# Kernel tuning notes

Measured on AMD Instinct MI355X. Metric: run time of the kernel, lower is better.

## Reference

```python
import jax, jax.numpy as jnp
import numpy as np
from math import sqrt

INPUT, HIDDEN, OUTPUT = 256, 512, 256
B, T = 64, 1024


def setup_inputs() -> dict:
    key = jax.random.key(0)
    k1, k2, k3, k4 = jax.random.split(key, 4)
    x = jax.random.normal(k1, (B, T, INPUT), dtype=jnp.float32)
    W_xh = jax.random.normal(k2, (INPUT, HIDDEN), dtype=jnp.float32) * sqrt(2.0 / (INPUT + HIDDEN))
    W_hh = jax.random.normal(k3, (HIDDEN, HIDDEN), dtype=jnp.float32) * sqrt(1.0 / HIDDEN)
    b_h = jnp.zeros((HIDDEN,), dtype=jnp.float32)
    W_hy = jax.random.normal(k4, (HIDDEN, OUTPUT), dtype=jnp.float32) * sqrt(2.0 / (HIDDEN + OUTPUT))
    b_y = jnp.zeros((OUTPUT,), dtype=jnp.float32)
    return {"x": x, "W_xh": W_xh, "W_hh": W_hh, "b_h": b_h, "W_hy": W_hy, "b_y": b_y}


def reference(x, W_xh, W_hh, b_h, W_hy, b_y):
    # Precompute input projection for all timesteps: [B,T,H_in] @ [H_in,H] -> [B,T,H]
    xh = jnp.einsum('bti,ih->bth', x, W_xh) + b_h
    h0 = jnp.zeros((x.shape[0], W_hh.shape[0]), dtype=x.dtype)

    def step(h, xh_t):
        h_new = jnp.tanh(h @ W_hh + xh_t)  # [B,H]
        return h_new, h_new

    # scan over time: xh transposed to [T,B,H]
    _, hs = jax.lax.scan(step, h0, jnp.swapaxes(xh, 0, 1))
    hs = jnp.swapaxes(hs, 0, 1)  # [B,T,H]
    outputs = jnp.einsum('bth,ho->bto', hs, W_hy) + b_y  # [B,T,O]
    return outputs
```

## Files before the change

kernel.cpp:

```cpp
#include <hip/hip_runtime.h>
#include <hip/hip_bf16.h>
#include <hip/hip_fp16.h>


#define BT 65536
#define HID 512
#define NIN 256
#define NOUT 256
#define TSTEPS 1024
#define NBATCH 64

typedef _Float16 hf2_t __attribute__((ext_vector_type(2)));

__device__ __forceinline__ float fdot2(unsigned w, unsigned h, float acc) {
#if __has_builtin(__builtin_amdgcn_fdot2)
    return __builtin_amdgcn_fdot2(__builtin_bit_cast(hf2_t, w),
                                  __builtin_bit_cast(hf2_t, h), acc, false);
#else
    __half2 wv = __builtin_bit_cast(__half2, w);
    __half2 hv = __builtin_bit_cast(__half2, h);
    float2 wf = __half22float2(wv);
    float2 hf = __half22float2(hv);
    return acc + wf.x * hf.x + wf.y * hf.y;
#endif
}

__device__ __forceinline__ float dot4(uint4 w, uint4 h, float acc) {
    acc = fdot2(w.x, h.x, acc);
    acc = fdot2(w.y, h.y, acc);
    acc = fdot2(w.z, h.z, acc);
    acc = fdot2(w.w, h.w, acc);
    return acc;
}

__device__ __forceinline__ unsigned pack2h(float a, float b) {
    unsigned lo = (unsigned)__half_as_ushort(__float2half_rn(a));
    unsigned hi = (unsigned)__half_as_ushort(__float2half_rn(b));
    return lo | (hi << 16);
}

template <int CTRL>
__device__ __forceinline__ float dpp_add(float x) {
    int y = __builtin_amdgcn_mov_dpp(__float_as_int(x), CTRL, 0xF, 0xF, true);
    return x + __int_as_float(y);
}
template <int CTRL>
__device__ __forceinline__ float dpp_get(float x) {
    int y = __builtin_amdgcn_mov_dpp(__float_as_int(x), CTRL, 0xF, 0xF, true);
    return __int_as_float(y);
}

__device__ __forceinline__ float fast_tanh(float x) {
    float e = __builtin_amdgcn_exp2f(x * 2.8853900817779268f);
    return 1.0f - 2.0f * __builtin_amdgcn_rcpf(e + 1.0f);
}

__device__ __forceinline__ float4 load4f(const float* p) {
    return *(const float4*)p;
}
__device__ __forceinline__ float4 load4f(const __half* p) {
    ushort4 u = *(const ushort4*)p;
    float4 r;
    r.x = __half2float(__ushort_as_half(u.x));
    r.y = __half2float(__ushort_as_half(u.y));
    r.z = __half2float(__ushort_as_half(u.z));
    r.w = __half2float(__ushort_as_half(u.w));
    return r;
}
__device__ __forceinline__ void store1(float* p, float v) { *p = v; }
__device__ __forceinline__ void store1(__half* p, float v) { *p = __float2half_rn(v); }

__global__ __launch_bounds__(256)
void pack_w_kernel(const float* __restrict__ W,
                   unsigned* __restrict__ reg_blob,
                   unsigned* __restrict__ gcol_blob) {
    int t = blockIdx.x;
    int w = threadIdx.x;
    int i = w >> 2, u = w & 3;
    int g = t >> 3, s = t & 7;
    int c = i >> 3, j = i & 7;
    int col = 8 * g + c;
    int k = 64 * s + 8 * j + 2 * u;
    unsigned val = pack2h(W[(size_t)k * HID + col], W[(size_t)(k + 1) * HID + col]);
    if (i < 48) reg_blob[(i * 512 + t) * 4 + u] = val;
    else        gcol_blob[((i - 48) * 512 + t) * 4 + u] = val;
}

template <typename AT, typename CT>
__global__ __launch_bounds__(256)
void gemm_bias_kernel(const AT* __restrict__ A, const float* __restrict__ B,
                      const float* __restrict__ bias, CT* __restrict__ C,
                      int M, int N, int K) {
    const int TM = 64, TN = 64, TK = 16;
    __shared__ float As[TK][TM];
    __shared__ float Bs[TK][TN + 4];

    int tid = threadIdx.x;
    int tx = tid & 15;
    int ty = tid >> 4;
    int row0 = blockIdx.x * TM;
    int col0 = blockIdx.y * TN;

    float c[4][4];
#pragma unroll
    for (int i = 0; i < 4; ++i)
#pragma unroll
        for (int j = 0; j < 4; ++j) c[i][j] = 0.f;

    for (int kk = 0; kk < K; kk += TK) {
        {
            int ar = tid >> 2;
            int ac = (tid & 3) * 4;
            float4 av = load4f(A + (size_t)(row0 + ar) * K + kk + ac);
            As[ac + 0][ar] = av.x;
            As[ac + 1][ar] = av.y;
            As[ac + 2][ar] = av.z;
            As[ac + 3][ar] = av.w;
        }
        {
            int br = tid >> 4;
            int bc = (tid & 15) * 4;
            float4 bv = *(const float4*)(B + (size_t)(kk + br) * N + col0 + bc);
            *(float4*)&Bs[br][bc] = bv;
        }
        __syncthreads();
#pragma unroll
        for (int k = 0; k < TK; ++k) {
            float4 a = *(const float4*)&As[k][ty * 4];
            float4 b = *(const float4*)&Bs[k][tx * 4];
            float av[4] = {a.x, a.y, a.z, a.w};
            float bv[4] = {b.x, b.y, b.z, b.w};
#pragma unroll
            for (int i = 0; i < 4; ++i)
#pragma unroll
                for (int j = 0; j < 4; ++j) c[i][j] += av[i] * bv[j];
        }
        __syncthreads();
    }

#pragma unroll
    for (int j = 0; j < 4; ++j) {
        float bb = bias[col0 + tx * 4 + j];
#pragma unroll
        for (int i = 0; i < 4; ++i) {
            int r = row0 + ty * 4 + i;
            int cc = col0 + tx * 4 + j;
            store1(&C[(size_t)r * N + cc], c[i][j] + bb);
        }
    }
}

template <typename AT, typename CT>
__global__ __launch_bounds__(256)
void gemm_bias_f16_kernel(const AT* __restrict__ A, const float* __restrict__ B,
                          const float* __restrict__ bias, CT* __restrict__ C,
                          int M, int N, int K) {
    const int TM = 64, TN = 64, TK = 16;
    __shared__ unsigned Asp[TK / 2][TM];
    __shared__ unsigned Bsp[TK / 2][TN + 4];

    int tid = threadIdx.x;
    int tx = tid & 15;
    int ty = tid >> 4;
    int row0 = blockIdx.x * TM;
    int col0 = blockIdx.y * TN;

    float c[4][4];
#pragma unroll
    for (int i = 0; i < 4; ++i)
#pragma unroll
        for (int j = 0; j < 4; ++j) c[i][j] = 0.f;

    for (int kk = 0; kk < K; kk += TK) {
        {
            int ar = tid >> 2;
            int ac = (tid & 3) * 4;
            float4 av = load4f(A + (size_t)(row0 + ar) * K + kk + ac);
            Asp[(ac >> 1) + 0][ar] = pack2h(av.x, av.y);
            Asp[(ac >> 1) + 1][ar] = pack2h(av.z, av.w);
        }
        {
            int k2 = tid >> 5;
            int bc = (tid & 31) * 2;
            const float* b0 = B + (size_t)(kk + 2 * k2) * N + col0 + bc;
            const float* b1 = b0 + N;
            float2 r0 = *(const float2*)b0;
            float2 r1 = *(const float2*)b1;
            Bsp[k2][bc + 0] = pack2h(r0.x, r1.x);
            Bsp[k2][bc + 1] = pack2h(r0.y, r1.y);
        }
        __syncthreads();
#pragma unroll
        for (int k2 = 0; k2 < TK / 2; ++k2) {
            uint4 ap = *(const uint4*)&Asp[k2][ty * 4];
            uint4 bp = *(const uint4*)&Bsp[k2][tx * 4];
            unsigned av[4] = {ap.x, ap.y, ap.z, ap.w};
            unsigned bv[4] = {bp.x, bp.y, bp.z, bp.w};
#pragma unroll
            for (int i = 0; i < 4; ++i)
#pragma unroll
                for (int j = 0; j < 4; ++j) c[i][j] = fdot2(av[i], bv[j], c[i][j]);
        }
        __syncthreads();
    }

#pragma unroll
    for (int j = 0; j < 4; ++j) {
        float bb = bias[col0 + tx * 4 + j];
#pragma unroll
        for (int i = 0; i < 4; ++i) {
            int r = row0 + ty * 4 + i;
            int cc = col0 + tx * 4 + j;
            store1(&C[(size_t)r * N + cc], c[i][j] + bb);
        }
    }
}

template <int GLN>
__global__ __launch_bounds__(512, 2)
void rnn_scan8(const __half* __restrict__ xh,
               const uint4* __restrict__ reg_blob,
               const uint4* __restrict__ gcol_blob,
               __half* __restrict__ hs) {
    __shared__ __align__(16) uint4 hbuf4[2][72];
    extern __shared__ __align__(16) uint4 gl_[];

    const int t = threadIdx.x;
    const int b = blockIdx.x;
    const int g = t >> 3, s = t & 7;

    uint4 W[48];
#pragma unroll
    for (int i = 0; i < 48; ++i) W[i] = reg_blob[i * 512 + t];
#pragma unroll
    for (int j = 0; j < GLN; ++j) gl_[j * 512 + t] = gcol_blob[j * 512 + t];

    if (t < 72) {
        hbuf4[0][t] = uint4{0u, 0u, 0u, 0u};
        hbuf4[1][t] = uint4{0u, 0u, 0u, 0u};
    }
    __syncthreads();

    const int col = 8 * g + s;
    const __half* xp = xh + (size_t)b * TSTEPS * HID + col;
    __half* hp = hs + (size_t)b * TSTEPS * HID + col;
    const uint4* gb = gcol_blob + t;

    const int H = col >> 1;
    const int wordC = ((H >> 5) * 9 + ((H >> 2) & 7)) * 4 + (H & 3);

#define GETG(j) (((j) < GLN) ? gl_[(j) * 512 + t] : gb[(size_t)(j) * 512])

    int cur = 0;
    __half prev = __ushort_as_half((unsigned short)0);

    for (int step = 0; step < TSTEPS; ++step) {
        float xv = __half2float(xp[(size_t)step * HID]);
        if (step) hp[(size_t)(step - 1) * HID] = prev;

        const uint4* hv = &hbuf4[cur][s * 9];
        float acc[8];
#pragma unroll
        for (int c = 0; c < 8; ++c) acc[c] = 0.f;

#pragma unroll
        for (int ch = 0; ch < 2; ++ch) {
            const int j4 = ch * 4;
            uint4 h0 = hv[j4 + 0];
            uint4 h1 = hv[j4 + 1];
            uint4 h2 = hv[j4 + 2];
            uint4 h3 = hv[j4 + 3];
#pragma unroll
            for (int c = 0; c < 6; ++c) {
                acc[c] = dot4(W[c * 8 + j4 + 0], h0, acc[c]);
                acc[c] = dot4(W[c * 8 + j4 + 1], h1, acc[c]);
                acc[c] = dot4(W[c * 8 + j4 + 2], h2, acc[c]);
                acc[c] = dot4(W[c * 8 + j4 + 3], h3, acc[c]);
            }
            {
                uint4 g0 = GETG(j4 + 0), g1 = GETG(j4 + 1);
                uint4 g2 = GETG(j4 + 2), g3 = GETG(j4 + 3);
                acc[6] = dot4(g0, h0, acc[6]); acc[6] = dot4(g1, h1, acc[6]);
                acc[6] = dot4(g2, h2, acc[6]); acc[6] = dot4(g3, h3, acc[6]);
            }
            {
                uint4 g0 = GETG(8 + j4 + 0), g1 = GETG(8 + j4 + 1);
                uint4 g2 = GETG(8 + j4 + 2), g3 = GETG(8 + j4 + 3);
                acc[7] = dot4(g0, h0, acc[7]); acc[7] = dot4(g1, h1, acc[7]);
                acc[7] = dot4(g2, h2, acc[7]); acc[7] = dot4(g3, h3, acc[7]);
            }
        }
#undef GETG

#pragma unroll
        for (int c = 0; c < 8; ++c) {
            acc[c] = dpp_add<0xB1>(acc[c]);
            acc[c] = dpp_add<0x4E>(acc[c]);
            acc[c] = dpp_add<0x141>(acc[c]);
        }

        float tot = acc[0];
        tot = (s == 1) ? acc[1] : tot;
        tot = (s == 2) ? acc[2] : tot;
        tot = (s == 3) ? acc[3] : tot;
        tot = (s == 4) ? acc[4] : tot;
        tot = (s == 5) ? acc[5] : tot;
        tot = (s == 6) ? acc[6] : tot;
        tot = (s == 7) ? acc[7] : tot;

        float hn = fast_tanh(tot + xv);
        prev = __float2half_rn(hn);

        float hi = dpp_get<0xB1>(hn);
        unsigned* hwp = (unsigned*)&hbuf4[cur ^ 1][0];
        if (!(s & 1)) hwp[wordC] = pack2h(hn, hi);
        __syncthreads();
        cur ^= 1;
    }
    hp[(size_t)(TSTEPS - 1) * HID] = prev;
}

extern "C" void kernel_launch(void* const* d_in, const int* in_sizes, int n_in,
                              void* d_out, int out_size, void* d_ws, size_t ws_size,
                              hipStream_t stream) {
    const float* x    = (const float*)d_in[0];
    const float* W_xh = (const float*)d_in[1];
    const float* W_hh = (const float*)d_in[2];
    const float* b_h  = (const float*)d_in[3];
    const float* W_hy = (const float*)d_in[4];
    const float* b_y  = (const float*)d_in[5];
    float* out = (float*)d_out;

    char* ws = (char*)d_ws;
    const size_t off_gcol = 48 * 512 * 16;
    const size_t off_xh   = (size_t)1 << 20;
    const size_t off_hs   = off_xh + (size_t)BT * HID * 2;

    unsigned* reg_blob  = (unsigned*)ws;
    unsigned* gcol_blob = (unsigned*)(ws + off_gcol);
    __half*   xh        = (__half*)(ws + off_xh);
    __half*   hs        = (__half*)(ws + off_hs);

    pack_w_kernel<<<dim3(512), dim3(256), 0, stream>>>(W_hh, reg_blob, gcol_blob);

    gemm_bias_kernel<float, __half>
        <<<dim3(BT / 64, HID / 64), dim3(256), 0, stream>>>(x, W_xh, b_h, xh, BT, HID, NIN);

    const int GL16_BYTES = 16 * 512 * 16;
    hipError_t e = hipFuncSetAttribute(
        reinterpret_cast<const void*>(&rnn_scan8<16>),
        hipFuncAttributeMaxDynamicSharedMemorySize, GL16_BYTES);
    if (e == hipSuccess) {
        rnn_scan8<16><<<dim3(NBATCH), dim3(512), GL16_BYTES, stream>>>(
            xh, (const uint4*)reg_blob, (const uint4*)gcol_blob, hs);
    } else {
        (void)hipGetLastError();
        rnn_scan8<7><<<dim3(NBATCH), dim3(512), 7 * 512 * 16, stream>>>(
            xh, (const uint4*)reg_blob, (const uint4*)gcol_blob, hs);
    }

    gemm_bias_f16_kernel<__half, float>
        <<<dim3(BT / 64, NOUT / 64), dim3(256), 0, stream>>>(hs, W_hy, b_y, out, BT, NOUT, HID);
}
```

Baseline: 1.869 ms.

## Restructure RNN scan inner loop and move half of gate columns to global

Replaces the chunked inner loop with one loop over 8 h-vectors, loading each h chunk once and feeding all 8 accumulators. Shrinks the LDS-resident weight columns from 16 to 8 slots, so the other 8 column slots are read from global or L2 every step. Swaps launch_bounds min-blocks for amdgpu_waves_per_eu(2,2) and adds a compiler memory barrier after the register weight loads. The aim is to change register pressure and load scheduling in the latency-bound recurrent step, at the cost of extra global traffic per step.

```diff
diff --git a/kernel.cpp b/kernel.cpp
--- a/kernel.cpp
+++ b/kernel.cpp
@@ -217,7 +217,8 @@
 }
 
 template <int GLN>
-__global__ __launch_bounds__(512, 2)
+__global__ __launch_bounds__(512)
+__attribute__((amdgpu_waves_per_eu(2, 2)))
 void rnn_scan8(const __half* __restrict__ xh,
                const uint4* __restrict__ reg_blob,
                const uint4* __restrict__ gcol_blob,
@@ -232,6 +233,8 @@
     uint4 W[48];
 #pragma unroll
     for (int i = 0; i < 48; ++i) W[i] = reg_blob[i * 512 + t];
+    asm volatile("" ::: "memory");
+
 #pragma unroll
     for (int j = 0; j < GLN; ++j) gl_[j * 512 + t] = gcol_blob[j * 512 + t];
 
@@ -264,31 +267,18 @@
         for (int c = 0; c < 8; ++c) acc[c] = 0.f;
 
 #pragma unroll
-        for (int ch = 0; ch < 2; ++ch) {
-            const int j4 = ch * 4;
-            uint4 h0 = hv[j4 + 0];
-            uint4 h1 = hv[j4 + 1];
-            uint4 h2 = hv[j4 + 2];
-            uint4 h3 = hv[j4 + 3];
-#pragma unroll
-            for (int c = 0; c < 6; ++c) {
-                acc[c] = dot4(W[c * 8 + j4 + 0], h0, acc[c]);
-                acc[c] = dot4(W[c * 8 + j4 + 1], h1, acc[c]);
-                acc[c] = dot4(W[c * 8 + j4 + 2], h2, acc[c]);
-                acc[c] = dot4(W[c * 8 + j4 + 3], h3, acc[c]);
-            }
-            {
-                uint4 g0 = GETG(j4 + 0), g1 = GETG(j4 + 1);
-                uint4 g2 = GETG(j4 + 2), g3 = GETG(j4 + 3);
-                acc[6] = dot4(g0, h0, acc[6]); acc[6] = dot4(g1, h1, acc[6]);
-                acc[6] = dot4(g2, h2, acc[6]); acc[6] = dot4(g3, h3, acc[6]);
-            }
-            {
-                uint4 g0 = GETG(8 + j4 + 0), g1 = GETG(8 + j4 + 1);
-                uint4 g2 = GETG(8 + j4 + 2), g3 = GETG(8 + j4 + 3);
-                acc[7] = dot4(g0, h0, acc[7]); acc[7] = dot4(g1, h1, acc[7]);
-                acc[7] = dot4(g2, h2, acc[7]); acc[7] = dot4(g3, h3, acc[7]);
-            }
+        for (int j = 0; j < 8; ++j) {
+            uint4 hj = hv[j];
+            uint4 gA = GETG(j);
+            uint4 gB = GETG(8 + j);
+            acc[0] = dot4(W[0 * 8 + j], hj, acc[0]);
+            acc[1] = dot4(W[1 * 8 + j], hj, acc[1]);
+            acc[2] = dot4(W[2 * 8 + j], hj, acc[2]);
+            acc[3] = dot4(W[3 * 8 + j], hj, acc[3]);
+            acc[4] = dot4(W[4 * 8 + j], hj, acc[4]);
+            acc[5] = dot4(W[5 * 8 + j], hj, acc[5]);
+            acc[6] = dot4(gA, hj, acc[6]);
+            acc[7] = dot4(gB, hj, acc[7]);
         }
 #undef GETG
 
@@ -346,12 +336,12 @@
     gemm_bias_kernel<float, __half>
         <<<dim3(BT / 64, HID / 64), dim3(256), 0, stream>>>(x, W_xh, b_h, xh, BT, HID, NIN);
 
-    const int GL16_BYTES = 16 * 512 * 16;
+    const int GLDS_BYTES = 8 * 512 * 16;
     hipError_t e = hipFuncSetAttribute(
-        reinterpret_cast<const void*>(&rnn_scan8<16>),
-        hipFuncAttributeMaxDynamicSharedMemorySize, GL16_BYTES);
+        reinterpret_cast<const void*>(&rnn_scan8<8>),
+        hipFuncAttributeMaxDynamicSharedMemorySize, GLDS_BYTES);
     if (e == hipSuccess) {
-        rnn_scan8<16><<<dim3(NBATCH), dim3(512), GL16_BYTES, stream>>>(
+        rnn_scan8<8><<<dim3(NBATCH), dim3(512), GLDS_BYTES, stream>>>(
             xh, (const uint4*)reg_blob, (const uint4*)gcol_blob, hs);
     } else {
         (void)hipGetLastError();
```

Result: slower. 2.012 ms (+7.7%).
